# Kernel optimization log

Measured on AMD Instinct MI355X. Metric: run time of the kernel, lower is better.

## Reference

```python
import jax, jax.numpy as jnp
import numpy as np

B, H, W, C = 32, 56, 56, 192
P, HEADS = 7, 6
HD = C // HEADS
SCALE = HD ** -0.5
EPS = 1e-5


def _rel_pos_index(p):
    coords = np.stack(np.meshgrid(np.arange(p), np.arange(p), indexing='ij')).reshape(2, -1)
    rel = (coords[:, :, None] - coords[:, None, :]).transpose(1, 2, 0).astype(np.int64)
    rel[:, :, 0] += p - 1
    rel[:, :, 1] += p - 1
    rel[:, :, 0] *= 2 * p - 1
    return rel.sum(-1)  # (p*p, p*p)

REL_IDX = jnp.asarray(_rel_pos_index(P))


def _ln(x, g, b):
    mu = x.mean(-1, keepdims=True)
    var = ((x - mu) ** 2).mean(-1, keepdims=True)
    return (x - mu) * jax.lax.rsqrt(var + EPS) * g + b


def setup_inputs():
    key = jax.random.key(0)
    ks = jax.random.split(key, 8)
    s = 0.02
    return {
        'x': jax.random.normal(ks[0], (B, H * W, C), jnp.float32),
        'norm1_g': jnp.ones((C,), jnp.float32),
        'norm1_b': jnp.zeros((C,), jnp.float32),
        'qkv_w': jax.random.normal(ks[1], (C, 3 * C), jnp.float32) * s,
        'qkv_b': jnp.zeros((3 * C,), jnp.float32),
        'rpe_table': jax.random.normal(ks[2], ((2 * P - 1) ** 2, HEADS), jnp.float32) * s,
        'proj_w': jax.random.normal(ks[3], (C, C), jnp.float32) * s,
        'proj_b': jnp.zeros((C,), jnp.float32),
        'norm2_g': jnp.ones((C,), jnp.float32),
        'norm2_b': jnp.zeros((C,), jnp.float32),
        'fc1_w': jax.random.normal(ks[4], (C, 4 * C), jnp.float32) * s,
        'fc1_b': jnp.zeros((4 * C,), jnp.float32),
        'fc2_w': jax.random.normal(ks[5], (4 * C, C), jnp.float32) * s,
        'fc2_b': jnp.zeros((C,), jnp.float32),
    }


def reference(x, norm1_g, norm1_b, qkv_w, qkv_b, rpe_table, proj_w, proj_b,
              norm2_g, norm2_b, fc1_w, fc1_b, fc2_w, fc2_b):
    N = P * P
    shortcut = x
    h = _ln(x, norm1_g, norm1_b).reshape(B, H, W, C)
    # partition -> (B*nH*nW, N, C)
    h = h.reshape(B, H // P, P, W // P, P, C).transpose(0, 1, 3, 2, 4, 5)
    patches = h.reshape(-1, N, C)
    B_ = patches.shape[0]
    # qkv
    qkv = (patches @ qkv_w + qkv_b).reshape(B_, N, 3, HEADS, HD)
    q, k, v = qkv[:, :, 0], qkv[:, :, 1], qkv[:, :, 2]  # (B_, N, HEADS, HD)
    attn = jnp.einsum('bnhd,bmhd->bhnm', q * SCALE, k)
    bias = rpe_table[REL_IDX.reshape(-1)].reshape(N, N, HEADS).transpose(2, 0, 1)
    attn = jax.nn.softmax(attn + bias[None], axis=-1)
    out = jnp.einsum('bhnm,bmhd->bnhd', attn, v).reshape(B_, N, C)
    out = out @ proj_w + proj_b
    # reverse -> (B, H*W, C)
    out = out.reshape(B, H // P, W // P, P, P, C).transpose(0, 1, 3, 2, 4, 5).reshape(B, H * W, C)
    x = shortcut + out
    h = _ln(x, norm2_g, norm2_b)
    h = jax.nn.gelu(h @ fc1_w + fc1_b, approximate=False) @ fc2_w + fc2_b
    return x + h
```

## Files before the change

kernel.cpp:

```cpp
#include <hip/hip_runtime.h>
#include <cstdint>

using u16 = unsigned short;
using u32 = unsigned int;

typedef __bf16 bf16x8 __attribute__((ext_vector_type(8)));
typedef float f32x4 __attribute__((ext_vector_type(4)));
typedef short short4v __attribute__((ext_vector_type(4)));

constexpr int TOK = 100352;
constexpr float LOG2E = 1.4426950408889634f;
constexpr float SCALE_QL = 0.25503490f;

__device__ __forceinline__ float bf2f(u16 u) {
  union { u32 i; float f; } z; z.i = ((u32)u) << 16; return z.f;
}
__device__ __forceinline__ u16 f2bf(float f) {
  union { float f; u32 i; } z; z.f = f;
  u32 r = z.i + 0x7FFFu + ((z.i >> 16) & 1u);
  return (u16)(r >> 16);
}
__device__ __forceinline__ u32 pk2bf(float a, float b) {
  union { __bf16 h[2]; u32 w; } z;
  z.h[0] = (__bf16)a; z.h[1] = (__bf16)b; return z.w;
}

__device__ __forceinline__ float gelu_f(float v) {
  float t = -v * (2.3022587f + 0.10294455f * v * v);
  float e = exp2f(t);
  return v * __builtin_amdgcn_rcpf(1.f + e);
}

__device__ __forceinline__ void gload_lds16(const void* g, void* l) {
  __builtin_amdgcn_global_load_lds((const __attribute__((address_space(1))) void*)g,
                                   (__attribute__((address_space(3))) void*)l, 16, 0, 0);
}

__global__ void transpose_pad(const float* __restrict__ src, u16* __restrict__ dst,
                              int N, int Npad, int K) {
  int id = blockIdx.x * 256 + threadIdx.x;
  if (id >= Npad * K) return;
  int n = id / K, k = id - n * K;
  float v = (n < N) ? src[(size_t)k * N + n] : 0.f;
  dst[id] = f2bf(v);
}

__global__ void transpose_swz1(const float* __restrict__ src, u16* __restrict__ dst) {
  int id = blockIdx.x * 256 + threadIdx.x;
  if (id >= 768 * 192) return;
  int n = id / 192, k = id - n * 192;
  int sg = (k >> 3) ^ (n & 7);
  dst[n * 192 + sg * 8 + (k & 7)] = f2bf(src[(size_t)k * 768 + n]);
}
__global__ void transpose_swz2(const float* __restrict__ src, u16* __restrict__ dst) {
  int id = blockIdx.x * 256 + threadIdx.x;
  if (id >= 192 * 768) return;
  int oc = id / 768, gc = id - oc * 768;
  int ch = gc >> 5, gcl = gc & 31;
  int f = gcl >> 4, gq = (gcl >> 2) & 3, e = gcl & 3;
  int P = oc * 4 + (gq ^ ((oc >> 2) & 3));
  dst[ch * 6144 + P * 8 + f * 4 + e] = f2bf(src[(size_t)gc * 192 + oc]);
}

template<int MODE>
__global__ __launch_bounds__(256) void ln_kernel(const float* __restrict__ x,
                                                 const u16* __restrict__ proj,
                                                 const float* __restrict__ g,
                                                 const float* __restrict__ b,
                                                 u16* __restrict__ out) {
  int row  = blockIdx.x * 4 + (threadIdx.x >> 6);
  int lane = threadIdx.x & 63;
  const float* xr = x + (size_t)row * 192;
  float v[3];
  #pragma unroll
  for (int t = 0; t < 3; ++t) {
    int c = lane + 64 * t;
    v[t] = xr[c];
    if (MODE == 1) v[t] += bf2f(proj[(size_t)row * 192 + c]);
  }
  float s = v[0] + v[1] + v[2];
  #pragma unroll
  for (int o = 32; o; o >>= 1) s += __shfl_xor(s, o);
  float mu = s * (1.f / 192.f);
  float q = 0.f;
  #pragma unroll
  for (int t = 0; t < 3; ++t) { float d = v[t] - mu; q += d * d; }
  #pragma unroll
  for (int o = 32; o; o >>= 1) q += __shfl_xor(q, o);
  float rs = rsqrtf(q * (1.f / 192.f) + 1e-5f);
  #pragma unroll
  for (int t = 0; t < 3; ++t) {
    int c = lane + 64 * t;
    out[(size_t)row * 192 + c] = f2bf((v[t] - mu) * rs * g[c] + b[c]);
  }
}

enum { MQKV = 0 };

template<int MODE, int MT, int NT, int N, int K, int LDC>
__global__ __launch_bounds__(256) void gemm_kernel(
    const u16* __restrict__ A, const u16* __restrict__ BT,
    const float* __restrict__ bias,
    u16* __restrict__ outb)
{
  constexpr int NWG = MT * NT;
  constexpr int NTL = K / 32;
  __shared__ __align__(16) u16 As[3][4096];
  __shared__ __align__(16) u16 Bs[3][4096];
  int tid = threadIdx.x;
  int wg = blockIdx.x;
  int lin = (wg & 7) * (NWG / 8) + (wg >> 3);
  int tileM = (lin / NT) * 128, tileN = (lin % NT) * 128;
  int lane = tid & 63, wave = tid >> 6;
  int wm = wave >> 1, wn = wave & 1;
  int g = lane >> 4, l15 = lane & 15;
  f32x4 acc[4][4] = {};

  int r0 = tid >> 2, kc = (tid & 3) * 8;
  const u16* Arow0 = A  + (size_t)(tileM + r0)      * K + kc;
  const u16* Arow1 = A  + (size_t)(tileM + r0 + 64) * K + kc;
  const u16* Brow0 = BT + (size_t)(tileN + r0)      * K + kc;
  const u16* Brow1 = BT + (size_t)(tileN + r0 + 64) * K + kc;
  const int wo = wave * 512;

#define GSTAGE(buf, k0) do {                              \
    gload_lds16(Arow0 + (k0), &As[buf][wo]);              \
    gload_lds16(Arow1 + (k0), &As[buf][2048 + wo]);       \
    gload_lds16(Brow0 + (k0), &Bs[buf][wo]);              \
    gload_lds16(Brow1 + (k0), &Bs[buf][2048 + wo]);       \
  } while (0)

  GSTAGE(0, 0);
  GSTAGE(1, 32);

  #pragma unroll
  for (int t = 0; t < NTL; ++t) {
    if (t + 1 < NTL) asm volatile("s_waitcnt vmcnt(4)" ::: "memory");
    else             asm volatile("s_waitcnt vmcnt(0)" ::: "memory");
    __builtin_amdgcn_s_barrier();
    __builtin_amdgcn_sched_barrier(0);
    if (t + 2 < NTL) GSTAGE((t + 2) % 3, (t + 2) * 32);
    const int cur = t % 3;
    bf16x8 af[4], bfr[4];
    #pragma unroll
    for (int mi = 0; mi < 4; ++mi)
      af[mi] = *(const bf16x8*)&As[cur][(wm * 64 + mi * 16 + l15) * 32 + g * 8];
    #pragma unroll
    for (int ni = 0; ni < 4; ++ni)
      bfr[ni] = *(const bf16x8*)&Bs[cur][(wn * 64 + ni * 16 + l15) * 32 + g * 8];
    #pragma unroll
    for (int mi = 0; mi < 4; ++mi)
      #pragma unroll
      for (int ni = 0; ni < 4; ++ni)
        acc[mi][ni] = __builtin_amdgcn_mfma_f32_16x16x32_bf16(bfr[ni], af[mi], acc[mi][ni], 0, 0, 0);
    __builtin_amdgcn_sched_barrier(0);
  }
#undef GSTAGE

  int cb = tileN + wn * 64 + g * 4;
  f32x4 bv4[4];
  bool cok[4];
  #pragma unroll
  for (int ni = 0; ni < 4; ++ni) {
    cok[ni] = (cb + ni * 16) < N;
    bv4[ni] = cok[ni] ? *(const f32x4*)&bias[cb + ni * 16] : f32x4{};
  }
  #pragma unroll
  for (int mi = 0; mi < 4; ++mi) {
    size_t row = (size_t)(tileM + wm * 64 + mi * 16 + l15);
    u16* orow = outb + row * LDC + cb;
    #pragma unroll
    for (int ni = 0; ni < 4; ++ni) {
      if (!cok[ni]) continue;
      float v0 = acc[mi][ni][0] + bv4[ni][0];
      float v1 = acc[mi][ni][1] + bv4[ni][1];
      float v2 = acc[mi][ni][2] + bv4[ni][2];
      float v3 = acc[mi][ni][3] + bv4[ni][3];
      if (MODE == MQKV && (cb + ni * 16) < 192) {
        v0 *= SCALE_QL; v1 *= SCALE_QL; v2 *= SCALE_QL; v3 *= SCALE_QL;
      }
      uint2 w;
      w.x = pk2bf(v0, v1);
      w.y = pk2bf(v2, v3);
      *(uint2*)&orow[ni * 16] = w;
    }
  }
}

__global__ __launch_bounds__(256, 2) void proj_ln(
    const u16* __restrict__ A,
    const u16* __restrict__ BT,
    const float* __restrict__ bias,
    const float* __restrict__ x,
    const float* __restrict__ n2g, const float* __restrict__ n2b,
    float* __restrict__ resid, u16* __restrict__ h2)
{
  constexpr int NWG = 784;
  __shared__ __align__(16) u16 As[3][4096];
  __shared__ __align__(16) u16 Bs[3][6144];
  int tid = threadIdx.x;
  int wg = blockIdx.x;
  int lin = (wg & 7) * (NWG / 8) + (wg >> 3);
  int tileM = lin * 128;
  int lane = tid & 63, wave = tid >> 6;
  int g = lane >> 4, l15 = lane & 15;
  f32x4 acc[2][12] = {};

  int r0 = tid >> 2, kc = (tid & 3) * 8;
  const u16* Arow0 = A + (size_t)(tileM + r0)      * 192 + kc;
  const u16* Arow1 = A + (size_t)(tileM + r0 + 64) * 192 + kc;
  const u16* Brow[3];
  #pragma unroll
  for (int i = 0; i < 3; ++i) {
    int s = (wave * 3 + i) * 64 + lane;
    Brow[i] = BT + (size_t)(s >> 2) * 192 + (s & 3) * 8;
  }
  const int wo = wave * 512;

#define PSTAGE(buf, k0) do {                                   \
    gload_lds16(Arow0 + (k0), &As[buf][wo]);                   \
    gload_lds16(Arow1 + (k0), &As[buf][2048 + wo]);            \
    _Pragma("unroll")                                          \
    for (int i = 0; i < 3; ++i)                                \
      gload_lds16(Brow[i] + (k0), &Bs[buf][(wave * 3 + i) * 512]); \
  } while (0)

  PSTAGE(0, 0);
  PSTAGE(1, 32);

  #pragma unroll
  for (int t = 0; t < 6; ++t) {
    if (t + 1 < 6) asm volatile("s_waitcnt vmcnt(5)" ::: "memory");
    else           asm volatile("s_waitcnt vmcnt(0)" ::: "memory");
    __builtin_amdgcn_s_barrier();
    __builtin_amdgcn_sched_barrier(0);
    if (t + 2 < 6) PSTAGE((t + 2) % 3, (t + 2) * 32);
    const int cur = t % 3;
    bf16x8 af[2], bfr[12];
    #pragma unroll
    for (int mi = 0; mi < 2; ++mi)
      af[mi] = *(const bf16x8*)&As[cur][(wave * 32 + mi * 16 + l15) * 32 + g * 8];
    #pragma unroll
    for (int ni = 0; ni < 12; ++ni)
      bfr[ni] = *(const bf16x8*)&Bs[cur][(ni * 16 + l15) * 32 + g * 8];
    #pragma unroll
    for (int mi = 0; mi < 2; ++mi)
      #pragma unroll
      for (int ni = 0; ni < 12; ++ni)
        acc[mi][ni] = __builtin_amdgcn_mfma_f32_16x16x32_bf16(bfr[ni], af[mi], acc[mi][ni], 0, 0, 0);
    __builtin_amdgcn_sched_barrier(0);
  }
#undef PSTAGE

  float s1[2] = {0.f, 0.f}, s2[2] = {0.f, 0.f};
  #pragma unroll
  for (int mi = 0; mi < 2; ++mi) {
    size_t row = (size_t)(tileM + wave * 32 + mi * 16 + l15);
    #pragma unroll
    for (int ni = 0; ni < 12; ++ni) {
      int cb = ni * 16 + g * 4;
      f32x4 bv = *(const f32x4*)&bias[cb];
      f32x4 xv = *(const f32x4*)&x[row * 192 + cb];
      f32x4 o;
      #pragma unroll
      for (int r = 0; r < 4; ++r) {
        o[r] = acc[mi][ni][r] + bv[r] + xv[r];
        s1[mi] += o[r];
        s2[mi] += o[r] * o[r];
      }
      acc[mi][ni] = o;
      *(f32x4*)&resid[row * 192 + cb] = o;
    }
  }
  #pragma unroll
  for (int mi = 0; mi < 2; ++mi) {
    s1[mi] += __shfl_xor(s1[mi], 16); s1[mi] += __shfl_xor(s1[mi], 32);
    s2[mi] += __shfl_xor(s2[mi], 16); s2[mi] += __shfl_xor(s2[mi], 32);
  }
  #pragma unroll
  for (int mi = 0; mi < 2; ++mi) {
    float mu = s1[mi] * (1.f / 192.f);
    float var = s2[mi] * (1.f / 192.f) - mu * mu;
    float rs = rsqrtf(var + 1e-5f);
    size_t row = (size_t)(tileM + wave * 32 + mi * 16 + l15);
    #pragma unroll
    for (int ni = 0; ni < 12; ++ni) {
      int cb = ni * 16 + g * 4;
      f32x4 gv = *(const f32x4*)&n2g[cb];
      f32x4 bv = *(const f32x4*)&n2b[cb];
      uint2 w;
      w.x = pk2bf((acc[mi][ni][0] - mu) * rs * gv[0] + bv[0],
                  (acc[mi][ni][1] - mu) * rs * gv[1] + bv[1]);
      w.y = pk2bf((acc[mi][ni][2] - mu) * rs * gv[2] + bv[2],
                  (acc[mi][ni][3] - mu) * rs * gv[3] + bv[3]);
      *(uint2*)&h2[row * 192 + cb] = w;
    }
  }
}

__global__ __launch_bounds__(256, 3) void mlp_fused(
    const u16* __restrict__ h2, const float* __restrict__ resid,
    const u16* __restrict__ w1g,
    const u16* __restrict__ w2g,
    const float* __restrict__ fc1b, const float* __restrict__ fc2b,
    float* __restrict__ out)
{
  __shared__ __align__(16) u16 W1c[2][6144];
  __shared__ __align__(16) u16 W2c[2][6144];
  __shared__ float B1s[768];
  __shared__ float B2s[192];

  int tid = threadIdx.x, lane = tid & 63, wave = tid >> 6;
  int g = lane >> 4, l15 = lane & 15;
  size_t row = (size_t)blockIdx.x * 64 + wave * 16 + l15;

  for (int c = tid; c < 768; c += 256) B1s[c] = fc1b[c];
  if (tid < 192) B2s[tid] = fc2b[tid];

  bf16x8 xf[6];
  #pragma unroll
  for (int ks = 0; ks < 6; ++ks)
    xf[ks] = *(const bf16x8*)&h2[row * 192 + ks * 32 + g * 8];

#define MSTAGE(c) do {                                                    \
    _Pragma("unroll")                                                     \
    for (int it = 0; it < 3; ++it) {                                      \
      int s = it * 256 + tid;                                             \
      gload_lds16(w1g + (size_t)(c) * 6144 + s * 8,                       \
                  &W1c[(c) & 1][(it * 256 + wave * 64) * 8]);             \
      gload_lds16(w2g + (size_t)(c) * 6144 + s * 8,                       \
                  &W2c[(c) & 1][(it * 256 + wave * 64) * 8]);             \
    }                                                                     \
  } while (0)

  MSTAGE(0);
  __syncthreads();

  f32x4 accO[12] = {};
  const int p2sw = g ^ ((l15 >> 2) & 3);

  #pragma unroll 2
  for (int c = 0; c < 24; ++c) {
    asm volatile("s_waitcnt vmcnt(0)" ::: "memory");
    __builtin_amdgcn_s_barrier();
    __builtin_amdgcn_sched_barrier(0);
    if (c + 1 < 24) MSTAGE(c + 1);
    const int bs = c & 1;

    f32x4 acc1[2] = {};
    #pragma unroll
    for (int ks = 0; ks < 6; ++ks) {
      #pragma unroll
      for (int f = 0; f < 2; ++f) {
        int rl = f * 16 + l15;
        int sg = (ks * 4 + g) ^ (rl & 7);
        bf16x8 wf = *(const bf16x8*)&W1c[bs][rl * 192 + sg * 8];
        acc1[f] = __builtin_amdgcn_mfma_f32_16x16x32_bf16(wf, xf[ks], acc1[f], 0, 0, 0);
      }
    }
    short4v bp[2];
    #pragma unroll
    for (int f = 0; f < 2; ++f) {
      f32x4 bv = *(const f32x4*)&B1s[c * 32 + f * 16 + g * 4];
      float p0 = gelu_f(acc1[f][0] + bv[0]);
      float p1 = gelu_f(acc1[f][1] + bv[1]);
      float p2 = gelu_f(acc1[f][2] + bv[2]);
      float p3 = gelu_f(acc1[f][3] + bv[3]);
      union { u32 w[2]; short4v v; } uu;
      uu.w[0] = pk2bf(p0, p1);
      uu.w[1] = pk2bf(p2, p3);
      bp[f] = uu.v;
    }
    #pragma unroll
    for (int n = 0; n < 12; ++n) {
      int oc = n * 16 + l15;
      int P = oc * 4 + p2sw;
      union { bf16x8 v8; short4v h[2]; } wu;
      wu.v8 = *(const bf16x8*)&W2c[bs][P * 8];
      accO[n] = __builtin_amdgcn_mfma_f32_16x16x16bf16_1k(wu.h[0], bp[0], accO[n], 0, 0, 0);
      accO[n] = __builtin_amdgcn_mfma_f32_16x16x16bf16_1k(wu.h[1], bp[1], accO[n], 0, 0, 0);
    }
    __builtin_amdgcn_sched_barrier(0);
  }
#undef MSTAGE

  const float* rrow = resid + row * 192;
  float*      orow = out + row * 192;
  #pragma unroll
  for (int n = 0; n < 12; ++n) {
    int cb = n * 16 + g * 4;
    f32x4 bv = *(const f32x4*)&B2s[cb];
    f32x4 rv = *(const f32x4*)&rrow[cb];
    f32x4 o;
    o[0] = accO[n][0] + bv[0] + rv[0];
    o[1] = accO[n][1] + bv[1] + rv[1];
    o[2] = accO[n][2] + bv[2] + rv[2];
    o[3] = accO[n][3] + bv[3] + rv[3];
    *(f32x4*)&orow[cb] = o;
  }
}

__global__ __launch_bounds__(384, 4) void attn_kernel(const u16* __restrict__ qkv,
                                                      const float* __restrict__ rpe,
                                                      u16* __restrict__ aout) {
  __shared__ __align__(16) u16 VT[192 * 72];
  __shared__ float RPE[1014];

  int tid = threadIdx.x;
  int win = blockIdx.x;
  int b = win >> 6, rem = win & 63, wh = rem >> 3, ww = rem & 7;
  const size_t wbase = (size_t)b * 3136 + (size_t)(wh * 7) * 56 + ww * 7;

  for (int c = tid; c < 1176; c += 384) {
    int dchunk = c / 49, tkn = c - dchunk * 49;
    int d0 = dchunk * 8;
    int yi = tkn / 7, xi = tkn - yi * 7;
    size_t t = wbase + yi * 56 + xi;
    uint4 v = *(const uint4*)&qkv[t * 576 + 384 + d0];
    const u16* e = (const u16*)&v;
    #pragma unroll
    for (int u = 0; u < 8; ++u) VT[(d0 + u) * 72 + tkn] = e[u];
  }
  for (int c = tid; c < 2880; c += 384) {
    int d = c / 15, n = 49 + (c - d * 15);
    VT[d * 72 + n] = 0;
  }
  for (int c = tid; c < 1014; c += 384) RPE[c] = rpe[c] * LOG2E;
  __syncthreads();

  int wave = tid >> 6, lane = tid & 63;
  int g = lane >> 4, l15 = lane & 15;
  int h = wave;

  bf16x8 afk[4], bfq[4];
  #pragma unroll
  for (int f = 0; f < 4; ++f) {
    int row = f * 16 + l15; row = min(row, 48);
    int y = row / 7, xx = row - y * 7;
    const u16* base = &qkv[(wbase + (size_t)y * 56 + xx) * 576];
    bfq[f] = *(const bf16x8*)(base + h * 32 + g * 8);
    afk[f] = *(const bf16x8*)(base + 192 + h * 32 + g * 8);
  }

  f32x4 acc[4][4] = {};
  __builtin_amdgcn_s_setprio(1);
  #pragma unroll
  for (int mj = 0; mj < 4; ++mj)
    #pragma unroll
    for (int ni = 0; ni < 4; ++ni)
      acc[mj][ni] = __builtin_amdgcn_mfma_f32_16x16x32_bf16(afk[mj], bfq[ni], acc[mj][ni], 0, 0, 0);
  __builtin_amdgcn_s_setprio(0);

  float sums[4];
  short4v bp[4][4];
  #pragma unroll
  for (int ni = 0; ni < 4; ++ni) {
    int i = ni * 16 + l15;
    int yi = i / 7, xi = i - yi * 7;
    #pragma unroll
    for (int mj = 0; mj < 4; ++mj)
      #pragma unroll
      for (int r = 0; r < 4; ++r) {
        int j = mj * 16 + g * 4 + r;
        int yj = j / 7, xj = j - yj * 7;
        int idx = (yi - yj + 6) * 13 + (xi - xj + 6);
        idx = max(0, min(idx, 168));
        float s = acc[mj][ni][r] + RPE[idx * 6 + h];
        acc[mj][ni][r] = (j < 49) ? s : -1e30f;
      }
    float m = -1e30f;
    #pragma unroll
    for (int mj = 0; mj < 4; ++mj) {
      f32x4 a = acc[mj][ni];
      m = fmaxf(m, fmaxf(fmaxf(a[0], a[1]), fmaxf(a[2], a[3])));
    }
    m = fmaxf(m, __shfl_xor(m, 16));
    m = fmaxf(m, __shfl_xor(m, 32));
    float sum = 0.f;
    #pragma unroll
    for (int mj = 0; mj < 4; ++mj) {
      float p0 = exp2f(acc[mj][ni][0] - m);
      float p1 = exp2f(acc[mj][ni][1] - m);
      float p2 = exp2f(acc[mj][ni][2] - m);
      float p3 = exp2f(acc[mj][ni][3] - m);
      sum += (p0 + p1) + (p2 + p3);
      union { u32 w[2]; short4v v; } uu;
      uu.w[0] = pk2bf(p0, p1);
      uu.w[1] = pk2bf(p2, p3);
      bp[ni][mj] = uu.v;
    }
    sum += __shfl_xor(sum, 16);
    sum += __shfl_xor(sum, 32);
    sums[ni] = sum;
  }

  f32x4 accO[2][4] = {};
  #pragma unroll
  for (int ks = 0; ks < 4; ++ks) {
    short4v av[2];
    #pragma unroll
    for (int md = 0; md < 2; ++md)
      av[md] = *(const short4v*)&VT[(h * 32 + md * 16 + l15) * 72 + ks * 16 + g * 4];
    __builtin_amdgcn_s_setprio(1);
    #pragma unroll
    for (int md = 0; md < 2; ++md)
      #pragma unroll
      for (int ni = 0; ni < 4; ++ni)
        accO[md][ni] = __builtin_amdgcn_mfma_f32_16x16x16bf16_1k(av[md], bp[ni][ks], accO[md][ni], 0, 0, 0);
    __builtin_amdgcn_s_setprio(0);
  }

  #pragma unroll
  for (int ni = 0; ni < 4; ++ni) {
    int i = ni * 16 + l15;
    if (i >= 49) continue;
    float inv = __builtin_amdgcn_rcpf(sums[ni]);
    int y = i / 7, xx = i - y * 7;
    u16* orow = &aout[(wbase + (size_t)y * 56 + xx) * 192 + h * 32];
    #pragma unroll
    for (int md = 0; md < 2; ++md) {
      int d0 = md * 16 + g * 4;
      *(u32*)&orow[d0]     = pk2bf(accO[md][ni][0] * inv, accO[md][ni][1] * inv);
      *(u32*)&orow[d0 + 2] = pk2bf(accO[md][ni][2] * inv, accO[md][ni][3] * inv);
    }
  }
}

extern "C" void kernel_launch(void* const* d_in, const int* in_sizes, int n_in,
                              void* d_out, int out_size, void* d_ws, size_t ws_size,
                              hipStream_t stream) {
  const float* x      = (const float*)d_in[0];
  const float* n1g    = (const float*)d_in[1];
  const float* n1b    = (const float*)d_in[2];
  const float* qkv_w  = (const float*)d_in[3];
  const float* qkv_b  = (const float*)d_in[4];
  const float* rpe    = (const float*)d_in[5];
  const float* proj_w = (const float*)d_in[6];
  const float* proj_b = (const float*)d_in[7];
  const float* n2g    = (const float*)d_in[8];
  const float* n2b    = (const float*)d_in[9];
  const float* fc1_w  = (const float*)d_in[10];
  const float* fc1_b  = (const float*)d_in[11];
  const float* fc2_w  = (const float*)d_in[12];
  const float* fc2_b  = (const float*)d_in[13];
  float* out = (float*)d_out;
  char* ws = (char*)d_ws;

  u16* qkvT  = (u16*)(ws + 0);
  u16* projT = (u16*)(ws + 245760);
  u16* fc1T  = (u16*)(ws + 344064);
  u16* fc2T  = (u16*)(ws + 638976);
  u16* ln1   = (u16*)(ws + 1048576);
  u16* qkvB  = (u16*)(ws + 39583744);
  float* resid = (float*)(ws + 78118912);
  u16* attnO = ln1;
  u16* h2    = qkvB;
  if (ws_size < 193724416u) return;

  transpose_pad<<<(640*192+255)/256, 256, 0, stream>>>(qkv_w,  qkvT, 576, 640, 192);
  transpose_pad<<<(256*192+255)/256, 256, 0, stream>>>(proj_w, projT, 192, 256, 192);
  transpose_swz1<<<576, 256, 0, stream>>>(fc1_w, fc1T);
  transpose_swz2<<<576, 256, 0, stream>>>(fc2_w, fc2T);

  ln_kernel<0><<<TOK/4, 256, 0, stream>>>(x, nullptr, n1g, n1b, ln1);

  gemm_kernel<MQKV, 784, 5, 576, 192, 576><<<3920, 256, 0, stream>>>(
      ln1, qkvT, qkv_b, qkvB);

  attn_kernel<<<2048, 384, 0, stream>>>(qkvB, rpe, attnO);

  proj_ln<<<784, 256, 0, stream>>>(
      attnO, projT, proj_b, x, n2g, n2b, resid, h2);

  mlp_fused<<<TOK/64, 256, 0, stream>>>(
      h2, resid, fc1T, fc2T, fc1_b, fc2_b, out);
}
```

Baseline: 340.1 us.

## Make QKV GEMM persistent over M tiles and triple-buffer MLP weight loads

The QKV GEMM now has each workgroup process four consecutive 128-row M tiles, with the K-loop pipeline running continuously across tile boundaries. Each tile's epilogue is issued mid-pipeline, which cuts the launch from 3920 to 980 workgroups and hides the prologue and epilogue cost behind loads. The fused MLP kernel moves from double to triple buffering of weight chunks with a partial vmcnt wait, so loads stay two chunks ahead. This raises LDS use and lowers occupancy from three to two blocks per CU. The XCD remap is also generalized for workgroup counts not divisible by eight.

```diff
diff --git a/kernel.cpp b/kernel.cpp
--- a/kernel.cpp
+++ b/kernel.cpp
@@ -62,9 +62,7 @@
   dst[ch * 6144 + P * 8 + f * 4 + e] = f2bf(src[(size_t)gc * 192 + oc]);
 }
 
-template<int MODE>
 __global__ __launch_bounds__(256) void ln_kernel(const float* __restrict__ x,
-                                                 const u16* __restrict__ proj,
                                                  const float* __restrict__ g,
                                                  const float* __restrict__ b,
                                                  u16* __restrict__ out) {
@@ -73,11 +71,7 @@
   const float* xr = x + (size_t)row * 192;
   float v[3];
   #pragma unroll
-  for (int t = 0; t < 3; ++t) {
-    int c = lane + 64 * t;
-    v[t] = xr[c];
-    if (MODE == 1) v[t] += bf2f(proj[(size_t)row * 192 + c]);
-  }
+  for (int t = 0; t < 3; ++t) v[t] = xr[lane + 64 * t];
   float s = v[0] + v[1] + v[2];
   #pragma unroll
   for (int o = 32; o; o >>= 1) s += __shfl_xor(s, o);
@@ -95,52 +89,92 @@
   }
 }
 
-enum { MQKV = 0 };
-
-template<int MODE, int MT, int NT, int N, int K, int LDC>
-__global__ __launch_bounds__(256) void gemm_kernel(
+template<int MGRP, int NT, int N, int K, int LDC, int MPB>
+__global__ __launch_bounds__(256) void qkv_gemm(
     const u16* __restrict__ A, const u16* __restrict__ BT,
     const float* __restrict__ bias,
     u16* __restrict__ outb)
 {
-  constexpr int NWG = MT * NT;
+  constexpr int NWG = MGRP * NT;
   constexpr int NTL = K / 32;
+  constexpr int TOT = MPB * NTL;
   __shared__ __align__(16) u16 As[3][4096];
   __shared__ __align__(16) u16 Bs[3][4096];
   int tid = threadIdx.x;
   int wg = blockIdx.x;
-  int lin = (wg & 7) * (NWG / 8) + (wg >> 3);
-  int tileM = (lin / NT) * 128, tileN = (lin % NT) * 128;
+  constexpr int q8 = NWG / 8, r8 = NWG % 8;
+  int xcd = wg & 7, sub = wg >> 3;
+  int lin = (xcd < r8 ? xcd * (q8 + 1) : r8 * (q8 + 1) + (xcd - r8) * q8) + sub;
+  int tileM0 = (lin / NT) * (128 * MPB), tileN = (lin % NT) * 128;
   int lane = tid & 63, wave = tid >> 6;
   int wm = wave >> 1, wn = wave & 1;
   int g = lane >> 4, l15 = lane & 15;
   f32x4 acc[4][4] = {};
 
   int r0 = tid >> 2, kc = (tid & 3) * 8;
-  const u16* Arow0 = A  + (size_t)(tileM + r0)      * K + kc;
-  const u16* Arow1 = A  + (size_t)(tileM + r0 + 64) * K + kc;
+  const u16* Abase = A  + (size_t)(tileM0 + r0) * K + kc;
   const u16* Brow0 = BT + (size_t)(tileN + r0)      * K + kc;
   const u16* Brow1 = BT + (size_t)(tileN + r0 + 64) * K + kc;
   const int wo = wave * 512;
 
-#define GSTAGE(buf, k0) do {                              \
-    gload_lds16(Arow0 + (k0), &As[buf][wo]);              \
-    gload_lds16(Arow1 + (k0), &As[buf][2048 + wo]);       \
-    gload_lds16(Brow0 + (k0), &Bs[buf][wo]);              \
-    gload_lds16(Brow1 + (k0), &Bs[buf][2048 + wo]);       \
+  int cb = tileN + wn * 64 + g * 4;
+  f32x4 bv4[4];
+  bool cok[4];
+  #pragma unroll
+  for (int ni = 0; ni < 4; ++ni) {
+    cok[ni] = (cb + ni * 16) < N;
+    bv4[ni] = cok[ni] ? *(const f32x4*)&bias[cb + ni * 16] : f32x4{};
+  }
+
+  auto epi = [&](int m) {
+    #pragma unroll
+    for (int mi = 0; mi < 4; ++mi) {
+      size_t row = (size_t)(tileM0 + m * 128 + wm * 64 + mi * 16 + l15);
+      u16* orow = outb + row * LDC + cb;
+      #pragma unroll
+      for (int ni = 0; ni < 4; ++ni) {
+        if (!cok[ni]) continue;
+        float v0 = acc[mi][ni][0] + bv4[ni][0];
+        float v1 = acc[mi][ni][1] + bv4[ni][1];
+        float v2 = acc[mi][ni][2] + bv4[ni][2];
+        float v3 = acc[mi][ni][3] + bv4[ni][3];
+        if ((cb + ni * 16) < 192) {
+          v0 *= SCALE_QL; v1 *= SCALE_QL; v2 *= SCALE_QL; v3 *= SCALE_QL;
+        }
+        uint2 w;
+        w.x = pk2bf(v0, v1);
+        w.y = pk2bf(v2, v3);
+        *(uint2*)&orow[ni * 16] = w;
+      }
+    }
+    #pragma unroll
+    for (int mi = 0; mi < 4; ++mi)
+      #pragma unroll
+      for (int ni = 0; ni < 4; ++ni)
+        acc[mi][ni] = f32x4{};
+  };
+
+#define GSTAGE(s) do {                                                      \
+    const int buf_ = (s) % 3;                                               \
+    const size_t ao_ = (size_t)((s) / NTL) * 128 * K + ((s) % NTL) * 32;    \
+    gload_lds16(Abase + ao_,                 &As[buf_][wo]);                \
+    gload_lds16(Abase + (size_t)64*K + ao_,  &As[buf_][2048 + wo]);         \
+    gload_lds16(Brow0 + ((s) % NTL) * 32,    &Bs[buf_][wo]);                \
+    gload_lds16(Brow1 + ((s) % NTL) * 32,    &Bs[buf_][2048 + wo]);         \
   } while (0)
 
-  GSTAGE(0, 0);
-  GSTAGE(1, 32);
-
-  #pragma unroll
-  for (int t = 0; t < NTL; ++t) {
-    if (t + 1 < NTL) asm volatile("s_waitcnt vmcnt(4)" ::: "memory");
+  GSTAGE(0);
+  GSTAGE(1);
+
+  #pragma unroll
+  for (int s = 0; s < TOT; ++s) {
+    if (s + 1 < TOT) asm volatile("s_waitcnt vmcnt(4)" ::: "memory");
     else             asm volatile("s_waitcnt vmcnt(0)" ::: "memory");
     __builtin_amdgcn_s_barrier();
     __builtin_amdgcn_sched_barrier(0);
-    if (t + 2 < NTL) GSTAGE((t + 2) % 3, (t + 2) * 32);
-    const int cur = t % 3;
+    if (s > 0 && (s % NTL) == 0) epi(s / NTL - 1);
+    if (s + 2 < TOT) GSTAGE(s + 2);
+    const int cur = s % 3;
     bf16x8 af[4], bfr[4];
     #pragma unroll
     for (int mi = 0; mi < 4; ++mi)
@@ -156,35 +190,7 @@
     __builtin_amdgcn_sched_barrier(0);
   }
 #undef GSTAGE
-
-  int cb = tileN + wn * 64 + g * 4;
-  f32x4 bv4[4];
-  bool cok[4];
-  #pragma unroll
-  for (int ni = 0; ni < 4; ++ni) {
-    cok[ni] = (cb + ni * 16) < N;
-    bv4[ni] = cok[ni] ? *(const f32x4*)&bias[cb + ni * 16] : f32x4{};
-  }
-  #pragma unroll
-  for (int mi = 0; mi < 4; ++mi) {
-    size_t row = (size_t)(tileM + wm * 64 + mi * 16 + l15);
-    u16* orow = outb + row * LDC + cb;
-    #pragma unroll
-    for (int ni = 0; ni < 4; ++ni) {
-      if (!cok[ni]) continue;
-      float v0 = acc[mi][ni][0] + bv4[ni][0];
-      float v1 = acc[mi][ni][1] + bv4[ni][1];
-      float v2 = acc[mi][ni][2] + bv4[ni][2];
-      float v3 = acc[mi][ni][3] + bv4[ni][3];
-      if (MODE == MQKV && (cb + ni * 16) < 192) {
-        v0 *= SCALE_QL; v1 *= SCALE_QL; v2 *= SCALE_QL; v3 *= SCALE_QL;
-      }
-      uint2 w;
-      w.x = pk2bf(v0, v1);
-      w.y = pk2bf(v2, v3);
-      *(uint2*)&orow[ni * 16] = w;
-    }
-  }
+  epi(MPB - 1);
 }
 
 __global__ __launch_bounds__(256, 2) void proj_ln(
@@ -298,24 +304,21 @@
   }
 }
 
-__global__ __launch_bounds__(256, 3) void mlp_fused(
+__global__ __launch_bounds__(256, 2) void mlp_fused(
     const u16* __restrict__ h2, const float* __restrict__ resid,
     const u16* __restrict__ w1g,
     const u16* __restrict__ w2g,
     const float* __restrict__ fc1b, const float* __restrict__ fc2b,
     float* __restrict__ out)
 {
-  __shared__ __align__(16) u16 W1c[2][6144];
-  __shared__ __align__(16) u16 W2c[2][6144];
+  __shared__ __align__(16) u16 W1c[3][6144];
+  __shared__ __align__(16) u16 W2c[3][6144];
   __shared__ float B1s[768];
   __shared__ float B2s[192];
 
   int tid = threadIdx.x, lane = tid & 63, wave = tid >> 6;
   int g = lane >> 4, l15 = lane & 15;
   size_t row = (size_t)blockIdx.x * 64 + wave * 16 + l15;
-
-  for (int c = tid; c < 768; c += 256) B1s[c] = fc1b[c];
-  if (tid < 192) B2s[tid] = fc2b[tid];
 
   bf16x8 xf[6];
   #pragma unroll
@@ -326,26 +329,32 @@
     _Pragma("unroll")                                                     \
     for (int it = 0; it < 3; ++it) {                                      \
       int s = it * 256 + tid;                                             \
-      gload_lds16(w1g + (size_t)(c) * 6144 + s * 8,                       \
-                  &W1c[(c) & 1][(it * 256 + wave * 64) * 8]);             \
-      gload_lds16(w2g + (size_t)(c) * 6144 + s * 8,                       \
-                  &W2c[(c) & 1][(it * 256 + wave * 64) * 8]);             \
+      gload_lds16(w1g + (size_t)(c) * 6144 + s * 8,                      \
+                  &W1c[(c) % 3][(it * 256 + wave * 64) * 8]);             \
+      gload_lds16(w2g + (size_t)(c) * 6144 + s * 8,                      \
+                  &W2c[(c) % 3][(it * 256 + wave * 64) * 8]);             \
     }                                                                     \
   } while (0)
 
   MSTAGE(0);
-  __syncthreads();
+  MSTAGE(1);
+  for (int c = tid; c < 768; c += 256) B1s[c] = fc1b[c];
+  if (tid < 192) B2s[tid] = fc2b[tid];
+  asm volatile("s_waitcnt lgkmcnt(0)" ::: "memory");
+  __builtin_amdgcn_s_barrier();
+  __builtin_amdgcn_sched_barrier(0);
 
   f32x4 accO[12] = {};
   const int p2sw = g ^ ((l15 >> 2) & 3);
 
-  #pragma unroll 2
+  #pragma unroll 3
   for (int c = 0; c < 24; ++c) {
-    asm volatile("s_waitcnt vmcnt(0)" ::: "memory");
+    if (c + 1 < 24) asm volatile("s_waitcnt vmcnt(6)" ::: "memory");
+    else            asm volatile("s_waitcnt vmcnt(0)" ::: "memory");
     __builtin_amdgcn_s_barrier();
     __builtin_amdgcn_sched_barrier(0);
-    if (c + 1 < 24) MSTAGE(c + 1);
-    const int bs = c & 1;
+    if (c + 2 < 24) MSTAGE(c + 2);
+    const int bs = c % 3;
 
     f32x4 acc1[2] = {};
     #pragma unroll
@@ -562,9 +571,9 @@
   transpose_swz1<<<576, 256, 0, stream>>>(fc1_w, fc1T);
   transpose_swz2<<<576, 256, 0, stream>>>(fc2_w, fc2T);
 
-  ln_kernel<0><<<TOK/4, 256, 0, stream>>>(x, nullptr, n1g, n1b, ln1);
-
-  gemm_kernel<MQKV, 784, 5, 576, 192, 576><<<3920, 256, 0, stream>>>(
+  ln_kernel<<<TOK/4, 256, 0, stream>>>(x, n1g, n1b, ln1);
+
+  qkv_gemm<196, 5, 576, 192, 576, 4><<<980, 256, 0, stream>>>(
       ln1, qkvT, qkv_b, qkvB);
 
   attn_kernel<<<2048, 384, 0, stream>>>(qkvB, rpe, attnO);
```

After: 373.6 us. +9.9%, slower.

## Process two 16-row tiles per wave in fused MLP to reuse LDS weight fragments

Applied to the files above, without the earlier changes.

The fused MLP kernel now runs 2 waves per block instead of 4, and each wave computes two 16-row sub-tiles. Each weight fragment read from LDS therefore feeds two MFMAs, halving LDS weight reads per unit of compute and doubling the per-wave MFMA work between barriers. The cost is higher register pressure (double accumulators and activations) and fewer waves per block, which reduces latency hiding. The unused MODE template of the LayerNorm kernel is also removed as cleanup.

```diff
diff --git a/kernel.cpp b/kernel.cpp
--- a/kernel.cpp
+++ b/kernel.cpp
@@ -62,9 +62,7 @@
   dst[ch * 6144 + P * 8 + f * 4 + e] = f2bf(src[(size_t)gc * 192 + oc]);
 }
 
-template<int MODE>
 __global__ __launch_bounds__(256) void ln_kernel(const float* __restrict__ x,
-                                                 const u16* __restrict__ proj,
                                                  const float* __restrict__ g,
                                                  const float* __restrict__ b,
                                                  u16* __restrict__ out) {
@@ -73,11 +71,7 @@
   const float* xr = x + (size_t)row * 192;
   float v[3];
   #pragma unroll
-  for (int t = 0; t < 3; ++t) {
-    int c = lane + 64 * t;
-    v[t] = xr[c];
-    if (MODE == 1) v[t] += bf2f(proj[(size_t)row * 192 + c]);
-  }
+  for (int t = 0; t < 3; ++t) v[t] = xr[lane + 64 * t];
   float s = v[0] + v[1] + v[2];
   #pragma unroll
   for (int o = 32; o; o >>= 1) s += __shfl_xor(s, o);
@@ -298,7 +292,7 @@
   }
 }
 
-__global__ __launch_bounds__(256, 3) void mlp_fused(
+__global__ __launch_bounds__(128, 2) void mlp_fused(
     const u16* __restrict__ h2, const float* __restrict__ resid,
     const u16* __restrict__ w1g,
     const u16* __restrict__ w2g,
@@ -312,31 +306,34 @@
 
   int tid = threadIdx.x, lane = tid & 63, wave = tid >> 6;
   int g = lane >> 4, l15 = lane & 15;
-  size_t row = (size_t)blockIdx.x * 64 + wave * 16 + l15;
-
-  for (int c = tid; c < 768; c += 256) B1s[c] = fc1b[c];
-  if (tid < 192) B2s[tid] = fc2b[tid];
-
-  bf16x8 xf[6];
-  #pragma unroll
-  for (int ks = 0; ks < 6; ++ks)
-    xf[ks] = *(const bf16x8*)&h2[row * 192 + ks * 32 + g * 8];
+  size_t rowA = (size_t)blockIdx.x * 64 + wave * 32 + l15;
+
+  for (int c = tid; c < 768; c += 128) B1s[c] = fc1b[c];
+  for (int c = tid; c < 192; c += 128) B2s[c] = fc2b[c];
+
+  bf16x8 xfA[6], xfB[6];
+  #pragma unroll
+  for (int ks = 0; ks < 6; ++ks) {
+    xfA[ks] = *(const bf16x8*)&h2[rowA * 192 + ks * 32 + g * 8];
+    xfB[ks] = *(const bf16x8*)&h2[(rowA + 16) * 192 + ks * 32 + g * 8];
+  }
 
 #define MSTAGE(c) do {                                                    \
     _Pragma("unroll")                                                     \
-    for (int it = 0; it < 3; ++it) {                                      \
-      int s = it * 256 + tid;                                             \
+    for (int it = 0; it < 6; ++it) {                                      \
+      int s = it * 128 + tid;                                             \
       gload_lds16(w1g + (size_t)(c) * 6144 + s * 8,                       \
-                  &W1c[(c) & 1][(it * 256 + wave * 64) * 8]);             \
+                  &W1c[(c) & 1][(it * 128 + wave * 64) * 8]);             \
       gload_lds16(w2g + (size_t)(c) * 6144 + s * 8,                       \
-                  &W2c[(c) & 1][(it * 256 + wave * 64) * 8]);             \
+                  &W2c[(c) & 1][(it * 128 + wave * 64) * 8]);             \
     }                                                                     \
   } while (0)
 
   MSTAGE(0);
   __syncthreads();
 
-  f32x4 accO[12] = {};
+  f32x4 accOA[12] = {};
+  f32x4 accOB[12] = {};
   const int p2sw = g ^ ((l15 >> 2) & 3);
 
   #pragma unroll 2
@@ -347,7 +344,7 @@
     if (c + 1 < 24) MSTAGE(c + 1);
     const int bs = c & 1;
 
-    f32x4 acc1[2] = {};
+    f32x4 acc1A[2] = {}, acc1B[2] = {};
     #pragma unroll
     for (int ks = 0; ks < 6; ++ks) {
       #pragma unroll
@@ -355,21 +352,34 @@
         int rl = f * 16 + l15;
         int sg = (ks * 4 + g) ^ (rl & 7);
         bf16x8 wf = *(const bf16x8*)&W1c[bs][rl * 192 + sg * 8];
-        acc1[f] = __builtin_amdgcn_mfma_f32_16x16x32_bf16(wf, xf[ks], acc1[f], 0, 0, 0);
+        acc1A[f] = __builtin_amdgcn_mfma_f32_16x16x32_bf16(wf, xfA[ks], acc1A[f], 0, 0, 0);
+        acc1B[f] = __builtin_amdgcn_mfma_f32_16x16x32_bf16(wf, xfB[ks], acc1B[f], 0, 0, 0);
       }
     }
-    short4v bp[2];
+    short4v bpA[2], bpB[2];
     #pragma unroll
     for (int f = 0; f < 2; ++f) {
       f32x4 bv = *(const f32x4*)&B1s[c * 32 + f * 16 + g * 4];
-      float p0 = gelu_f(acc1[f][0] + bv[0]);
-      float p1 = gelu_f(acc1[f][1] + bv[1]);
-      float p2 = gelu_f(acc1[f][2] + bv[2]);
-      float p3 = gelu_f(acc1[f][3] + bv[3]);
-      union { u32 w[2]; short4v v; } uu;
-      uu.w[0] = pk2bf(p0, p1);
-      uu.w[1] = pk2bf(p2, p3);
-      bp[f] = uu.v;
+      {
+        float p0 = gelu_f(acc1A[f][0] + bv[0]);
+        float p1 = gelu_f(acc1A[f][1] + bv[1]);
+        float p2 = gelu_f(acc1A[f][2] + bv[2]);
+        float p3 = gelu_f(acc1A[f][3] + bv[3]);
+        union { u32 w[2]; short4v v; } uu;
+        uu.w[0] = pk2bf(p0, p1);
+        uu.w[1] = pk2bf(p2, p3);
+        bpA[f] = uu.v;
+      }
+      {
+        float p0 = gelu_f(acc1B[f][0] + bv[0]);
+        float p1 = gelu_f(acc1B[f][1] + bv[1]);
+        float p2 = gelu_f(acc1B[f][2] + bv[2]);
+        float p3 = gelu_f(acc1B[f][3] + bv[3]);
+        union { u32 w[2]; short4v v; } uu;
+        uu.w[0] = pk2bf(p0, p1);
+        uu.w[1] = pk2bf(p2, p3);
+        bpB[f] = uu.v;
+      }
     }
     #pragma unroll
     for (int n = 0; n < 12; ++n) {
@@ -377,26 +387,33 @@
       int P = oc * 4 + p2sw;
       union { bf16x8 v8; short4v h[2]; } wu;
       wu.v8 = *(const bf16x8*)&W2c[bs][P * 8];
-      accO[n] = __builtin_amdgcn_mfma_f32_16x16x16bf16_1k(wu.h[0], bp[0], accO[n], 0, 0, 0);
-      accO[n] = __builtin_amdgcn_mfma_f32_16x16x16bf16_1k(wu.h[1], bp[1], accO[n], 0, 0, 0);
+      accOA[n] = __builtin_amdgcn_mfma_f32_16x16x16bf16_1k(wu.h[0], bpA[0], accOA[n], 0, 0, 0);
+      accOA[n] = __builtin_amdgcn_mfma_f32_16x16x16bf16_1k(wu.h[1], bpA[1], accOA[n], 0, 0, 0);
+      accOB[n] = __builtin_amdgcn_mfma_f32_16x16x16bf16_1k(wu.h[0], bpB[0], accOB[n], 0, 0, 0);
+      accOB[n] = __builtin_amdgcn_mfma_f32_16x16x16bf16_1k(wu.h[1], bpB[1], accOB[n], 0, 0, 0);
     }
     __builtin_amdgcn_sched_barrier(0);
   }
 #undef MSTAGE
 
-  const float* rrow = resid + row * 192;
-  float*      orow = out + row * 192;
-  #pragma unroll
-  for (int n = 0; n < 12; ++n) {
-    int cb = n * 16 + g * 4;
-    f32x4 bv = *(const f32x4*)&B2s[cb];
-    f32x4 rv = *(const f32x4*)&rrow[cb];
-    f32x4 o;
-    o[0] = accO[n][0] + bv[0] + rv[0];
-    o[1] = accO[n][1] + bv[1] + rv[1];
-    o[2] = accO[n][2] + bv[2] + rv[2];
-    o[3] = accO[n][3] + bv[3] + rv[3];
-    *(f32x4*)&orow[cb] = o;
+  #pragma unroll
+  for (int half = 0; half < 2; ++half) {
+    size_t row = rowA + half * 16;
+    const f32x4* accO = half ? accOB : accOA;
+    const float* rrow = resid + row * 192;
+    float*      orow = out + row * 192;
+    #pragma unroll
+    for (int n = 0; n < 12; ++n) {
+      int cb = n * 16 + g * 4;
+      f32x4 bv = *(const f32x4*)&B2s[cb];
+      f32x4 rv = *(const f32x4*)&rrow[cb];
+      f32x4 o;
+      o[0] = accO[n][0] + bv[0] + rv[0];
+      o[1] = accO[n][1] + bv[1] + rv[1];
+      o[2] = accO[n][2] + bv[2] + rv[2];
+      o[3] = accO[n][3] + bv[3] + rv[3];
+      *(f32x4*)&orow[cb] = o;
+    }
   }
 }
 
@@ -562,7 +579,7 @@
   transpose_swz1<<<576, 256, 0, stream>>>(fc1_w, fc1T);
   transpose_swz2<<<576, 256, 0, stream>>>(fc2_w, fc2T);
 
-  ln_kernel<0><<<TOK/4, 256, 0, stream>>>(x, nullptr, n1g, n1b, ln1);
+  ln_kernel<<<TOK/4, 256, 0, stream>>>(x, n1g, n1b, ln1);
 
   gemm_kernel<MQKV, 784, 5, 576, 192, 576><<<3920, 256, 0, stream>>>(
       ln1, qkvT, qkv_b, qkvB);
@@ -572,6 +589,6 @@
   proj_ln<<<784, 256, 0, stream>>>(
       attnO, projT, proj_b, x, n2g, n2b, resid, h2);
 
-  mlp_fused<<<TOK/64, 256, 0, stream>>>(
+  mlp_fused<<<TOK/64, 128, 0, stream>>>(
       h2, resid, fc1T, fc2T, fc1_b, fc2_b, out);
 }
```

Result: slower. 371.7 us (+9.3%).
